# Optimization experiments

Measured on AMD Instinct MI355X. Metric: run time of the kernel, lower is better.

## Reference

```python
import jax, jax.numpy as jnp
import numpy as np

NUM_LAYERS = 3
CHANNELS = 8
IN_CHANNELS = 8
MASK_FEAT_STRIDE = 8
MASK_OUT_STRIDE = 4
FACTOR = MASK_FEAT_STRIDE // MASK_OUT_STRIDE  # 2

# param split sizes (weights first, then biases), matching parse_dynamic_params
W0 = (IN_CHANNELS + 2) * CHANNELS  # 80
W1 = CHANNELS * CHANNELS           # 64
W2 = CHANNELS * 1                  # 8
B0 = CHANNELS
B1 = CHANNELS
B2 = 1
NUM_GEN_PARAMS = W0 + W1 + W2 + B0 + B1 + B2  # 169


def compute_locations(h, w, stride):
    # matches adet.utils.comm.compute_locations: centers of stride-cells, (x, y)
    sx = jnp.arange(w, dtype=jnp.float32) * stride + stride // 2
    sy = jnp.arange(h, dtype=jnp.float32) * stride + stride // 2
    yy, xx = jnp.meshgrid(sy, sx, indexing='ij')
    return jnp.stack([xx.reshape(-1), yy.reshape(-1)], axis=1)  # [H*W, 2]


def _interp_axis_align(x, out_size, axis):
    # 1D bilinear with align_corners=True along `axis`
    in_size = x.shape[axis]
    pos = jnp.arange(out_size, dtype=jnp.float32) * ((in_size - 1) / (out_size - 1))
    i0 = jnp.floor(pos).astype(jnp.int32)
    i1 = jnp.minimum(i0 + 1, in_size - 1)
    w1 = (pos - i0.astype(jnp.float32)).astype(x.dtype)
    shape = [1] * x.ndim
    shape[axis] = out_size
    w1 = w1.reshape(shape)
    x0 = jnp.take(x, i0, axis=axis)
    x1 = jnp.take(x, i1, axis=axis)
    return x0 * (1 - w1) + x1 * w1


def aligned_bilinear(t, factor):
    # matches adet.utils.comm.aligned_bilinear
    if factor == 1:
        return t
    h, w = t.shape[2], t.shape[3]
    t = jnp.pad(t, ((0, 0), (0, 0), (0, 1), (0, 1)), mode='edge')
    oh, ow = factor * h + 1, factor * w + 1
    t = _interp_axis_align(t, oh, 2)
    t = _interp_axis_align(t, ow, 3)
    pad = factor // 2
    t = jnp.pad(t, ((0, 0), (0, 0), (pad, 0), (pad, 0)), mode='edge')
    return t[:, :, :oh - 1, :ow - 1]  # [N, C, factor*h, factor*w]


def setup_inputs() -> dict:
    key = jax.random.key(0)
    k1, k2, k3, k4, k5 = jax.random.split(key, 5)
    N, H, W = 2, 128, 192
    n_inst = 128
    mask_feats = jax.random.normal(k1, (N, IN_CHANNELS, H, W), dtype=jnp.float32)
    mask_head_params = jax.random.normal(k2, (n_inst, NUM_GEN_PARAMS), dtype=jnp.float32) * 0.1
    instance_locations = jax.random.uniform(k3, (n_inst, 2), dtype=jnp.float32) * 1024.0
    sizes_of_interest = jnp.array([64.0, 128.0, 256.0, 512.0, 1e8, 2e8], dtype=jnp.float32)
    im_inds = jax.random.randint(k4, (n_inst,), 0, N, dtype=jnp.int32)
    fpn_levels = jax.random.randint(k5, (n_inst,), 0, 5, dtype=jnp.int32)
    return {
        'mask_feats': mask_feats,
        'mask_head_params': mask_head_params,
        'instance_locations': instance_locations,
        'sizes_of_interest': sizes_of_interest,
        'im_inds': im_inds,
        'fpn_levels': fpn_levels,
    }


def reference(mask_feats, mask_head_params, instance_locations, sizes_of_interest, im_inds, fpn_levels):
    N, C, H, W = mask_feats.shape
    n = mask_head_params.shape[0]
    HW = H * W

    locs = compute_locations(H, W, MASK_FEAT_STRIDE)                 # [HW, 2]
    rel = instance_locations[:, None, :] - locs[None, :, :]          # [n, HW, 2]
    rel = jnp.transpose(rel, (0, 2, 1))                              # [n, 2, HW]
    soi = sizes_of_interest[fpn_levels]                              # [n]
    rel = rel / soi[:, None, None]

    feats = mask_feats[im_inds].reshape(n, C, HW)                    # gather per-instance image feats
    x = jnp.concatenate([rel, feats], axis=1)                        # [n, C+2, HW]

    p = mask_head_params
    w0 = p[:, :W0].reshape(n, CHANNELS, IN_CHANNELS + 2)
    w1 = p[:, W0:W0 + W1].reshape(n, CHANNELS, CHANNELS)
    w2 = p[:, W0 + W1:W0 + W1 + W2].reshape(n, 1, CHANNELS)
    off = W0 + W1 + W2
    b0 = p[:, off:off + B0]
    b1 = p[:, off + B0:off + B0 + B1]
    b2 = p[:, off + B0 + B1:off + B0 + B1 + B2]

    # per-instance dynamic 1x1-conv MLP (grouped conv == batched matmul)
    x = jax.nn.relu(jnp.einsum('noi,nip->nop', w0, x) + b0[:, :, None])
    x = jax.nn.relu(jnp.einsum('noi,nip->nop', w1, x) + b1[:, :, None])
    x = jnp.einsum('noi,nip->nop', w2, x) + b2[:, :, None]           # [n, 1, HW]

    mask_logits = x.reshape(n, 1, H, W)
    return aligned_bilinear(mask_logits, FACTOR)                     # [n, 1, 2H, 2W]
```

## Files before the change

### kernel.cpp

```cpp
#include <hip/hip_runtime.h>
#include <hip/hip_bf16.h>

#define NUM_INST 128
#define H_ 128
#define W_ 192
#define HW_ (H_ * W_)
#define OH_ 256
#define OW_ 384
#define NPAR 169

static __device__ __forceinline__ float bf2f(unsigned short u) {
    union { unsigned int i; float f; } v;
    v.i = ((unsigned int)u) << 16;
    return v.f;
}

static __device__ __forceinline__ unsigned int f2bf(float f) {
    unsigned int u = __float_as_uint(f);
    return (u + 0x7fffu + ((u >> 16) & 1u)) >> 16;
}

__global__ __launch_bounds__(256) void fused_maskhead(
    const void* __restrict__ mf_v,
    const void* __restrict__ par_v,
    const void* __restrict__ loc_v,
    const void* __restrict__ soi_v,
    const int*  __restrict__ im_inds,
    const int*  __restrict__ fpn,
    void*       __restrict__ out_v)
{
    const int tid  = threadIdx.x;
    const int inst = blockIdx.y;
    const int r0   = blockIdx.x * 8;

    const bool f32in = (*(const unsigned int*)soi_v) == 0x42800000u;

    __shared__ float w[NPAR];
    __shared__ float Lt[9][W_ + 1];

    if (tid < NPAR) {
        w[tid] = f32in ? ((const float*)par_v)[inst * NPAR + tid]
                       : bf2f(((const unsigned short*)par_v)[inst * NPAR + tid]);
    }

    float lx, ly, soi;
    const int lvl = fpn[inst];
    if (f32in) {
        lx  = ((const float*)loc_v)[inst * 2 + 0];
        ly  = ((const float*)loc_v)[inst * 2 + 1];
        soi = ((const float*)soi_v)[lvl];
    } else {
        lx  = bf2f(((const unsigned short*)loc_v)[inst * 2 + 0]);
        ly  = bf2f(((const unsigned short*)loc_v)[inst * 2 + 1]);
        soi = bf2f(((const unsigned short*)soi_v)[lvl]);
    }
    const float invs = 1.0f / soi;
    const size_t fo  = (size_t)im_inds[inst] * 8 * HW_;

    __syncthreads();

    for (int g = tid; g < 432; g += 256) {
        const int j  = g / 48;
        const int c0 = (g - j * 48) * 4;
        int rr = r0 - 1 + j; if (rr < 0) rr = 0;
        const int poff = rr * W_ + c0;

        float x[10][4];
        const float dy = (ly - (float)(rr * 8 + 4)) * invs;
#pragma unroll
        for (int k = 0; k < 4; k++) {
            x[0][k] = (lx - (float)((c0 + k) * 8 + 4)) * invs;
            x[1][k] = dy;
        }
        if (f32in) {
            const float* fb = (const float*)mf_v + fo + poff;
#pragma unroll
            for (int ch = 0; ch < 8; ch++) {
                float4 f = *(const float4*)(fb + ch * HW_);
                x[2 + ch][0] = f.x; x[2 + ch][1] = f.y;
                x[2 + ch][2] = f.z; x[2 + ch][3] = f.w;
            }
        } else {
            const unsigned short* fb = (const unsigned short*)mf_v + fo + poff;
#pragma unroll
            for (int ch = 0; ch < 8; ch++) {
                ushort4 f = *(const ushort4*)(fb + ch * HW_);
                x[2 + ch][0] = bf2f(f.x); x[2 + ch][1] = bf2f(f.y);
                x[2 + ch][2] = bf2f(f.z); x[2 + ch][3] = bf2f(f.w);
            }
        }

        float h1[8][4];
#pragma unroll
        for (int o = 0; o < 8; o++) {
            const float b = w[152 + o];
            float a0 = b, a1 = b, a2 = b, a3 = b;
#pragma unroll
            for (int i = 0; i < 10; i++) {
                const float wv = w[o * 10 + i];
                a0 = fmaf(wv, x[i][0], a0);
                a1 = fmaf(wv, x[i][1], a1);
                a2 = fmaf(wv, x[i][2], a2);
                a3 = fmaf(wv, x[i][3], a3);
            }
            h1[o][0] = fmaxf(a0, 0.0f); h1[o][1] = fmaxf(a1, 0.0f);
            h1[o][2] = fmaxf(a2, 0.0f); h1[o][3] = fmaxf(a3, 0.0f);
        }

        float h2[8][4];
#pragma unroll
        for (int o = 0; o < 8; o++) {
            const float b = w[160 + o];
            float a0 = b, a1 = b, a2 = b, a3 = b;
#pragma unroll
            for (int i = 0; i < 8; i++) {
                const float wv = w[80 + o * 8 + i];
                a0 = fmaf(wv, h1[i][0], a0);
                a1 = fmaf(wv, h1[i][1], a1);
                a2 = fmaf(wv, h1[i][2], a2);
                a3 = fmaf(wv, h1[i][3], a3);
            }
            h2[o][0] = fmaxf(a0, 0.0f); h2[o][1] = fmaxf(a1, 0.0f);
            h2[o][2] = fmaxf(a2, 0.0f); h2[o][3] = fmaxf(a3, 0.0f);
        }

        const float b2 = w[168];
        float o0 = b2, o1 = b2, o2 = b2, o3 = b2;
#pragma unroll
        for (int i = 0; i < 8; i++) {
            const float wv = w[144 + i];
            o0 = fmaf(wv, h2[i][0], o0);
            o1 = fmaf(wv, h2[i][1], o1);
            o2 = fmaf(wv, h2[i][2], o2);
            o3 = fmaf(wv, h2[i][3], o3);
        }

        Lt[j][c0 + 0] = o0; Lt[j][c0 + 1] = o1;
        Lt[j][c0 + 2] = o2; Lt[j][c0 + 3] = o3;
    }

    __syncthreads();

    for (int q = tid; q < 1536; q += 256) {
        const int rl = q / 192;
        const int c  = q - rl * 192;
        const int r  = r0 + rl;
        const int cm = c ? c - 1 : 0;

        const float a = Lt[rl][cm],     b = Lt[rl][c];
        const float d = Lt[rl + 1][cm], e = Lt[rl + 1][c];

        const float v00 = 0.25f * (a + b + d + e);
        const float v01 = 0.5f  * (b + e);
        const float v10 = 0.5f  * (d + e);
        const float v11 = e;

        const size_t base = ((size_t)inst * OH_ + 2 * r) * (size_t)OW_ + 2 * c;
        if (f32in) {
            float* of = (float*)out_v;
            *(float2*)(of + base)        = make_float2(v00, v01);
            *(float2*)(of + base + OW_)  = make_float2(v10, v11);
        } else {
            unsigned int* ob = (unsigned int*)out_v;
            ob[base >> 1]          = f2bf(v00) | (f2bf(v01) << 16);
            ob[(base + OW_) >> 1]  = f2bf(v10) | (f2bf(v11) << 16);
        }
    }
}

extern "C" void kernel_launch(void* const* d_in, const int* in_sizes, int n_in,
                              void* d_out, int out_size, void* d_ws, size_t ws_size,
                              hipStream_t stream) {
    (void)in_sizes; (void)n_in; (void)d_ws; (void)ws_size; (void)out_size;
    const void* mask_feats = d_in[0];
    const void* params     = d_in[1];
    const void* inst_loc   = d_in[2];
    const void* soi_tab    = d_in[3];
    const int*  im_inds    = (const int*)d_in[4];
    const int*  fpn_levels = (const int*)d_in[5];

    dim3 grid(H_ / 8, NUM_INST);
    fused_maskhead<<<grid, 256, 0, stream>>>(mask_feats, params, inst_loc,
                                             soi_tab, im_inds, fpn_levels, d_out);
}
```

Baseline: 98.66 us.

## Process eight columns per thread with hoisted coordinate terms and wider stores

Each thread now computes eight adjacent low-res pixels instead of four, in a single pass with no loop, so 216 of 256 threads are active. The thread uses wider 16-byte feature loads and folds the bias and y-coordinate term into one per-output constant. The upsampling stage handles two source columns per thread and writes 16-byte float4 or 8-byte packed bf16 stores, with float4 writes into padded shared memory. A launch-bounds occupancy hint is added. The larger per-thread register tile (h1 of 8x8) raises register pressure and may hurt occupancy.

```diff
diff --git a/kernel.cpp b/kernel.cpp
--- a/kernel.cpp
+++ b/kernel.cpp
@@ -1,5 +1,4 @@
 #include <hip/hip_runtime.h>
-#include <hip/hip_bf16.h>
 
 #define NUM_INST 128
 #define H_ 128
@@ -8,19 +7,25 @@
 #define OH_ 256
 #define OW_ 384
 #define NPAR 169
+#define LTS 196
 
 static __device__ __forceinline__ float bf2f(unsigned short u) {
     union { unsigned int i; float f; } v;
     v.i = ((unsigned int)u) << 16;
     return v.f;
 }
-
+static __device__ __forceinline__ float bflo(unsigned int d) {
+    union { unsigned int i; float f; } v; v.i = d << 16; return v.f;
+}
+static __device__ __forceinline__ float bfhi(unsigned int d) {
+    union { unsigned int i; float f; } v; v.i = d & 0xffff0000u; return v.f;
+}
 static __device__ __forceinline__ unsigned int f2bf(float f) {
     unsigned int u = __float_as_uint(f);
     return (u + 0x7fffu + ((u >> 16) & 1u)) >> 16;
 }
 
-__global__ __launch_bounds__(256) void fused_maskhead(
+__global__ __launch_bounds__(256, 4) void fused_maskhead(
     const void* __restrict__ mf_v,
     const void* __restrict__ par_v,
     const void* __restrict__ loc_v,
@@ -36,7 +41,7 @@
     const bool f32in = (*(const unsigned int*)soi_v) == 0x42800000u;
 
     __shared__ float w[NPAR];
-    __shared__ float Lt[9][W_ + 1];
+    __shared__ __align__(16) float Lt[9][LTS];
 
     if (tid < NPAR) {
         w[tid] = f32in ? ((const float*)par_v)[inst * NPAR + tid]
@@ -59,111 +64,147 @@
 
     __syncthreads();
 
-    for (int g = tid; g < 432; g += 256) {
-        const int j  = g / 48;
-        const int c0 = (g - j * 48) * 4;
+    if (tid < 216) {
+        const int j  = tid / 24;
+        const int c0 = (tid - j * 24) * 8;
         int rr = r0 - 1 + j; if (rr < 0) rr = 0;
         const int poff = rr * W_ + c0;
 
-        float x[10][4];
         const float dy = (ly - (float)(rr * 8 + 4)) * invs;
-#pragma unroll
-        for (int k = 0; k < 4; k++) {
-            x[0][k] = (lx - (float)((c0 + k) * 8 + 4)) * invs;
-            x[1][k] = dy;
+        float cx[8];
+#pragma unroll
+        for (int k = 0; k < 8; k++)
+            cx[k] = (lx - (float)((c0 + k) * 8 + 4)) * invs;
+
+        float h1[8][8];
+        if (!f32in) {
+            uint4 u[8];
+            const unsigned short* fb = (const unsigned short*)mf_v + fo + poff;
+#pragma unroll
+            for (int ch = 0; ch < 8; ch++)
+                u[ch] = *(const uint4*)(fb + ch * HW_);
+
+#pragma unroll
+            for (int o = 0; o < 8; o++) {
+                const float t  = fmaf(w[o * 10 + 1], dy, w[152 + o]);
+                const float wx = w[o * 10 + 0];
+#pragma unroll
+                for (int k = 0; k < 8; k++) h1[o][k] = fmaf(wx, cx[k], t);
+            }
+#pragma unroll
+            for (int ch = 0; ch < 8; ch++) {
+                float g[8];
+                g[0] = bflo(u[ch].x); g[1] = bfhi(u[ch].x);
+                g[2] = bflo(u[ch].y); g[3] = bfhi(u[ch].y);
+                g[4] = bflo(u[ch].z); g[5] = bfhi(u[ch].z);
+                g[6] = bflo(u[ch].w); g[7] = bfhi(u[ch].w);
+#pragma unroll
+                for (int o = 0; o < 8; o++) {
+                    const float wv = w[o * 10 + 2 + ch];
+#pragma unroll
+                    for (int k = 0; k < 8; k++)
+                        h1[o][k] = fmaf(wv, g[k], h1[o][k]);
+                }
+            }
+        } else {
+            const float* fb = (const float*)mf_v + fo + poff;
+#pragma unroll
+            for (int o = 0; o < 8; o++) {
+                const float t  = fmaf(w[o * 10 + 1], dy, w[152 + o]);
+                const float wx = w[o * 10 + 0];
+#pragma unroll
+                for (int k = 0; k < 8; k++) h1[o][k] = fmaf(wx, cx[k], t);
+            }
+#pragma unroll
+            for (int ch = 0; ch < 8; ch++) {
+                const float4 a = *(const float4*)(fb + ch * HW_);
+                const float4 b = *(const float4*)(fb + ch * HW_ + 4);
+                const float g[8] = {a.x, a.y, a.z, a.w, b.x, b.y, b.z, b.w};
+#pragma unroll
+                for (int o = 0; o < 8; o++) {
+                    const float wv = w[o * 10 + 2 + ch];
+#pragma unroll
+                    for (int k = 0; k < 8; k++)
+                        h1[o][k] = fmaf(wv, g[k], h1[o][k]);
+                }
+            }
         }
-        if (f32in) {
-            const float* fb = (const float*)mf_v + fo + poff;
-#pragma unroll
-            for (int ch = 0; ch < 8; ch++) {
-                float4 f = *(const float4*)(fb + ch * HW_);
-                x[2 + ch][0] = f.x; x[2 + ch][1] = f.y;
-                x[2 + ch][2] = f.z; x[2 + ch][3] = f.w;
-            }
-        } else {
-            const unsigned short* fb = (const unsigned short*)mf_v + fo + poff;
-#pragma unroll
-            for (int ch = 0; ch < 8; ch++) {
-                ushort4 f = *(const ushort4*)(fb + ch * HW_);
-                x[2 + ch][0] = bf2f(f.x); x[2 + ch][1] = bf2f(f.y);
-                x[2 + ch][2] = bf2f(f.z); x[2 + ch][3] = bf2f(f.w);
-            }
+#pragma unroll
+        for (int o = 0; o < 8; o++)
+#pragma unroll
+            for (int k = 0; k < 8; k++)
+                h1[o][k] = fmaxf(h1[o][k], 0.0f);
+
+#pragma unroll
+        for (int half = 0; half < 2; half++) {
+            float h2[8][4];
+#pragma unroll
+            for (int o = 0; o < 8; o++) {
+                const float b = w[160 + o];
+                float a0 = b, a1 = b, a2 = b, a3 = b;
+#pragma unroll
+                for (int i = 0; i < 8; i++) {
+                    const float wv = w[80 + o * 8 + i];
+                    a0 = fmaf(wv, h1[i][4 * half + 0], a0);
+                    a1 = fmaf(wv, h1[i][4 * half + 1], a1);
+                    a2 = fmaf(wv, h1[i][4 * half + 2], a2);
+                    a3 = fmaf(wv, h1[i][4 * half + 3], a3);
+                }
+                h2[o][0] = fmaxf(a0, 0.0f); h2[o][1] = fmaxf(a1, 0.0f);
+                h2[o][2] = fmaxf(a2, 0.0f); h2[o][3] = fmaxf(a3, 0.0f);
+            }
+            const float b2 = w[168];
+            float o0 = b2, o1 = b2, o2 = b2, o3 = b2;
+#pragma unroll
+            for (int i = 0; i < 8; i++) {
+                const float wv = w[144 + i];
+                o0 = fmaf(wv, h2[i][0], o0);
+                o1 = fmaf(wv, h2[i][1], o1);
+                o2 = fmaf(wv, h2[i][2], o2);
+                o3 = fmaf(wv, h2[i][3], o3);
+            }
+            *(float4*)&Lt[j][c0 + 4 * half] = make_float4(o0, o1, o2, o3);
         }
-
-        float h1[8][4];
-#pragma unroll
-        for (int o = 0; o < 8; o++) {
-            const float b = w[152 + o];
-            float a0 = b, a1 = b, a2 = b, a3 = b;
-#pragma unroll
-            for (int i = 0; i < 10; i++) {
-                const float wv = w[o * 10 + i];
-                a0 = fmaf(wv, x[i][0], a0);
-                a1 = fmaf(wv, x[i][1], a1);
-                a2 = fmaf(wv, x[i][2], a2);
-                a3 = fmaf(wv, x[i][3], a3);
-            }
-            h1[o][0] = fmaxf(a0, 0.0f); h1[o][1] = fmaxf(a1, 0.0f);
-            h1[o][2] = fmaxf(a2, 0.0f); h1[o][3] = fmaxf(a3, 0.0f);
-        }
-
-        float h2[8][4];
-#pragma unroll
-        for (int o = 0; o < 8; o++) {
-            const float b = w[160 + o];
-            float a0 = b, a1 = b, a2 = b, a3 = b;
-#pragma unroll
-            for (int i = 0; i < 8; i++) {
-                const float wv = w[80 + o * 8 + i];
-                a0 = fmaf(wv, h1[i][0], a0);
-                a1 = fmaf(wv, h1[i][1], a1);
-                a2 = fmaf(wv, h1[i][2], a2);
-                a3 = fmaf(wv, h1[i][3], a3);
-            }
-            h2[o][0] = fmaxf(a0, 0.0f); h2[o][1] = fmaxf(a1, 0.0f);
-            h2[o][2] = fmaxf(a2, 0.0f); h2[o][3] = fmaxf(a3, 0.0f);
-        }
-
-        const float b2 = w[168];
-        float o0 = b2, o1 = b2, o2 = b2, o3 = b2;
-#pragma unroll
-        for (int i = 0; i < 8; i++) {
-            const float wv = w[144 + i];
-            o0 = fmaf(wv, h2[i][0], o0);
-            o1 = fmaf(wv, h2[i][1], o1);
-            o2 = fmaf(wv, h2[i][2], o2);
-            o3 = fmaf(wv, h2[i][3], o3);
-        }
-
-        Lt[j][c0 + 0] = o0; Lt[j][c0 + 1] = o1;
-        Lt[j][c0 + 2] = o2; Lt[j][c0 + 3] = o3;
     }
 
     __syncthreads();
 
-    for (int q = tid; q < 1536; q += 256) {
-        const int rl = q / 192;
-        const int c  = q - rl * 192;
+#pragma unroll
+    for (int it = 0; it < 3; it++) {
+        const int q  = tid + it * 256;
+        const int rl = q / 96;
+        const int t  = q - rl * 96;
+        const int c2 = t * 2;
         const int r  = r0 + rl;
-        const int cm = c ? c - 1 : 0;
-
-        const float a = Lt[rl][cm],     b = Lt[rl][c];
-        const float d = Lt[rl + 1][cm], e = Lt[rl + 1][c];
-
-        const float v00 = 0.25f * (a + b + d + e);
-        const float v01 = 0.5f  * (b + e);
-        const float v10 = 0.5f  * (d + e);
-        const float v11 = e;
-
-        const size_t base = ((size_t)inst * OH_ + 2 * r) * (size_t)OW_ + 2 * c;
+        const int cm = c2 ? c2 - 1 : 0;
+
+        const float  am = Lt[rl][cm];
+        const float2 A  = *(const float2*)&Lt[rl][c2];
+        const float  dm = Lt[rl + 1][cm];
+        const float2 D  = *(const float2*)&Lt[rl + 1][c2];
+
+        const float v00 = 0.25f * (am + A.x + dm + D.x);
+        const float v01 = 0.5f  * (A.x + D.x);
+        const float v02 = 0.25f * (A.x + A.y + D.x + D.y);
+        const float v03 = 0.5f  * (A.y + D.y);
+        const float v10 = 0.5f  * (dm + D.x);
+        const float v11 = D.x;
+        const float v12 = 0.5f  * (D.x + D.y);
+        const float v13 = D.y;
+
+        const size_t base = ((size_t)inst * OH_ + 2 * r) * (size_t)OW_ + 2 * c2;
         if (f32in) {
             float* of = (float*)out_v;
-            *(float2*)(of + base)        = make_float2(v00, v01);
-            *(float2*)(of + base + OW_)  = make_float2(v10, v11);
+            *(float4*)(of + base)       = make_float4(v00, v01, v02, v03);
+            *(float4*)(of + base + OW_) = make_float4(v10, v11, v12, v13);
         } else {
             unsigned int* ob = (unsigned int*)out_v;
-            ob[base >> 1]          = f2bf(v00) | (f2bf(v01) << 16);
-            ob[(base + OW_) >> 1]  = f2bf(v10) | (f2bf(v11) << 16);
+            const unsigned int p0 = f2bf(v00) | (f2bf(v01) << 16);
+            const unsigned int p1 = f2bf(v02) | (f2bf(v03) << 16);
+            const unsigned int p2 = f2bf(v10) | (f2bf(v11) << 16);
+            const unsigned int p3 = f2bf(v12) | (f2bf(v13) << 16);
+            *(uint2*)(ob + (base >> 1))         = make_uint2(p0, p1);
+            *(uint2*)(ob + ((base + OW_) >> 1)) = make_uint2(p2, p3);
         }
     }
 }
```

Result: slower. 197.4 us (+100.1%).
